# Optimization experiments

Hardware: AMD Instinct MI355X
Metric: run time of the kernel (lower is better)

Reference implementation:

```python
import jax, jax.numpy as jnp
import numpy as np

TAU = 2.0          # LIF membrane time constant (init kwarg)
ALPHA = 2.0        # spikingjelly surrogate.ATan default alpha
V_TH = 1.0         # spikingjelly LIFNode default v_threshold

# Heaviside spike with ATan surrogate gradient (spikingjelly semantics)
@jax.custom_vjp
def spike(v):
    return (v >= V_TH).astype(v.dtype)

def _spike_fwd(v):
    return spike(v), v

def _spike_bwd(v, g):
    sg = (ALPHA / 2.0) / (1.0 + (jnp.pi / 2.0 * ALPHA * (v - V_TH)) ** 2)
    return (g * sg,)

spike.defvjp(_spike_fwd, _spike_bwd)

def lif(x):
    # Fresh LIFNode: v_prev = 0, v_reset = 0, decay_input=True
    # charge: v = v_prev + (x - (v_prev - v_reset)) / tau  ->  v = x / tau
    return spike(x / TAU)

def setup_inputs() -> dict:
    key = jax.random.key(0)
    ks = jax.random.split(key, 5)
    B = 2097152
    # kaiming-uniform-ish scale: 1/sqrt(fan_in)
    def w(k, out_f, in_f):
        return jax.random.normal(k, (out_f, in_f), dtype=jnp.float32) / np.sqrt(in_f)
    return {
        "x": jax.random.normal(ks[0], (B, 5), dtype=jnp.float32),
        "W1": w(ks[1], 32, 5),
        "W2": w(ks[2], 32, 32),
        "W3": w(ks[3], 16, 32),
        "W4": w(ks[4], 10, 16),
    }

def reference(x, W1, W2, W3, W4):
    # fc: Linear(5,32)->LIF -> Linear(32,32)->LIF -> Linear(32,16)->LIF
    s = lif(x @ W1.T)          # [B, 32]
    s = lif(s @ W2.T)          # [B, 32]
    s = lif(s @ W3.T)          # [B, 16]
    # fc1: Linear(16,10)->LIF
    return lif(s @ W4.T)       # [B, 10]
```

## Files before the change

### kernel.cpp

```cpp
#include <hip/hip_runtime.h>


typedef float v4f __attribute__((ext_vector_type(4)));

#define RPB 256

__global__ __launch_bounds__(256, 8) void snn_fused(
    const float* __restrict__ x,
    const float* __restrict__ W1,
    const float* __restrict__ W2,
    const float* __restrict__ W3,
    const float* __restrict__ W4,
    float* __restrict__ out,
    int B)
{
    __shared__ __align__(16) float xbuf[RPB * 5];
    __shared__ __align__(16) float obuf[RPB * 10];
    __shared__ float smx[32];
    __shared__ float smxmax;

    const int t = threadIdx.x;
    const long base = (long)blockIdx.x * RPB;
    const int nrows = (int)min((long)RPB, (long)B - base);

    if (t < 32) {
        float mm = W2[t];
#pragma unroll
        for (int j = 1; j < 32; ++j) mm = fmaxf(mm, W2[j * 32 + t]);
        smx[t] = mm;
        float r = mm;
#pragma unroll
        for (int off = 16; off; off >>= 1) r = fmaxf(r, __shfl_xor(r, off, 32));
        if (t == 0) smxmax = r;
    }

    if (nrows == RPB) {
        const v4f* xg = (const v4f*)(x + base * 5);
        v4f* b4 = (v4f*)xbuf;
#pragma unroll
        for (int e = 0; e < 2; ++e) {
            int idx = e * 256 + t;
            if (idx < (RPB * 5) / 4) b4[idx] = xg[idx];
        }
    } else {
        for (int e = t; e < nrows * 5; e += 256) xbuf[e] = x[base * 5 + e];
    }
    __syncthreads();

    const float mxmax = smxmax;

    if (t < nrows) {
        float xr[5];
#pragma unroll
        for (int k = 0; k < 5; ++k) xr[k] = xbuf[t * 5 + k];

        unsigned m = 0u;
#pragma unroll
        for (int j = 0; j < 32; ++j) {
            const float* w = W1 + j * 5;
            float h = xr[0] * w[0];
            h += xr[1] * w[1];
            h += xr[2] * w[2];
            h += xr[3] * w[3];
            h += xr[4] * w[4];
            if (h >= 2.0f) m |= (1u << j);
        }

        float o[10];
#pragma unroll
        for (int j = 0; j < 10; ++j) o[j] = 0.0f;

        if ((float)__popc(m) * mxmax >= 1.998f) {
            float S = 0.0f;
            unsigned mm = m;
            while (mm) { int i = __ffs(mm) - 1; mm &= mm - 1; S += smx[i]; }
            if (S >= 1.998f) {
                float h2[32];
#pragma unroll
                for (int j = 0; j < 32; ++j) h2[j] = 0.0f;
                mm = m;
                while (mm) {
                    int i = __ffs(mm) - 1;
                    mm &= mm - 1;
                    const float* col = W2 + i;
#pragma unroll
                    for (int j = 0; j < 32; ++j) h2[j] += col[j * 32];
                }
                unsigned m2 = 0u;
#pragma unroll
                for (int j = 0; j < 32; ++j)
                    if (h2[j] >= 2.0f) m2 |= (1u << j);

                if (m2) {
                    unsigned m3 = 0u;
#pragma unroll
                    for (int j = 0; j < 16; ++j) {
                        float g = 0.0f;
#pragma unroll
                        for (int i = 0; i < 32; ++i)
                            if ((m2 >> i) & 1u) g += W3[j * 32 + i];
                        if (g >= 2.0f) m3 |= (1u << j);
                    }
#pragma unroll
                    for (int j = 0; j < 10; ++j) {
                        float g = 0.0f;
#pragma unroll
                        for (int i = 0; i < 16; ++i)
                            if ((m3 >> i) & 1u) g += W4[j * 16 + i];
                        o[j] = (g >= 2.0f) ? 1.0f : 0.0f;
                    }
                }
            }
        }

#pragma unroll
        for (int j = 0; j < 10; ++j) obuf[t * 10 + j] = o[j];
    }
    __syncthreads();

    if (nrows == RPB) {
        v4f* og = (v4f*)(out + base * 10);
        const v4f* b4 = (const v4f*)obuf;
#pragma unroll
        for (int e = 0; e < 3; ++e) {
            int idx = e * 256 + t;
            if (idx < (RPB * 10) / 4)
                __builtin_nontemporal_store(b4[idx], &og[idx]);
        }
    } else {
        for (int e = t; e < nrows * 10; e += 256) out[base * 10 + e] = obuf[e];
    }
}

extern "C" void kernel_launch(void* const* d_in, const int* in_sizes, int n_in,
                              void* d_out, int out_size, void* d_ws, size_t ws_size,
                              hipStream_t stream) {
    const float* x  = (const float*)d_in[0];
    const float* W1 = (const float*)d_in[1];
    const float* W2 = (const float*)d_in[2];
    const float* W3 = (const float*)d_in[3];
    const float* W4 = (const float*)d_in[4];
    float* out = (float*)d_out;

    int B = in_sizes[0] / 5;
    int grid = (B + RPB - 1) / RPB;
    snn_fused<<<grid, 256, 0, stream>>>(x, W1, W2, W3, W4, out, B);
}
```

Before: 156.7 us.

## Process four rows per thread with prep kernel and wave-level shuffle screening

Adds a tiny prep kernel that transposes W1 into a workspace and precomputes per-column maxima of W2, so each main block no longer recomputes them. The main kernel now has each thread handle four rows, loaded and stored directly with vector accesses, replacing the shared-memory staging and both __syncthreads. Layer 1 uses packed float2 multiply-adds. The S screening sum uses wave-wide shuffles instead of shared-memory lookups. The costs are an extra kernel launch, higher register pressure, and fewer threads in flight with four times fewer blocks.

```diff
diff --git a/kernel.cpp b/kernel.cpp
--- a/kernel.cpp
+++ b/kernel.cpp
@@ -2,85 +2,109 @@
 
 
 typedef float v4f __attribute__((ext_vector_type(4)));
+typedef float v2f __attribute__((ext_vector_type(2)));
 
-#define RPB 256
+#define TPB 256
+#define RPL 4
+#define RPB (TPB * RPL)
 
-__global__ __launch_bounds__(256, 8) void snn_fused(
+__global__ __launch_bounds__(64) void snn_prep(
+    const float* __restrict__ W1,
+    const float* __restrict__ W2,
+    float* __restrict__ ws)
+{
+    const int t = threadIdx.x;
+    float mm = -3.4e38f;
+    if (t < 32) {
+#pragma unroll
+        for (int k = 0; k < 5; ++k) ws[k * 32 + t] = W1[t * 5 + k];
+        mm = W2[t];
+#pragma unroll
+        for (int j = 1; j < 32; ++j) mm = fmaxf(mm, W2[j * 32 + t]);
+        ws[160 + t] = mm;
+    }
+#pragma unroll
+    for (int off = 32; off; off >>= 1) mm = fmaxf(mm, __shfl_xor(mm, off));
+    if (t == 0) ws[192] = mm;
+}
+
+__global__ __launch_bounds__(TPB) void snn_fused(
     const float* __restrict__ x,
-    const float* __restrict__ W1,
     const float* __restrict__ W2,
     const float* __restrict__ W3,
     const float* __restrict__ W4,
+    const float* __restrict__ ws,
     float* __restrict__ out,
     int B)
 {
-    __shared__ __align__(16) float xbuf[RPB * 5];
-    __shared__ __align__(16) float obuf[RPB * 10];
-    __shared__ float smx[32];
-    __shared__ float smxmax;
+    const long gtid = (long)blockIdx.x * TPB + threadIdx.x;
+    const long r0 = gtid * RPL;
+    if (r0 >= B) return;
+    const bool full = (r0 + RPL <= B);
 
-    const int t = threadIdx.x;
-    const long base = (long)blockIdx.x * RPB;
-    const int nrows = (int)min((long)RPB, (long)B - base);
+    const v2f* __restrict__ w1p = (const v2f*)ws;
+    const float smxv = ws[160 + (threadIdx.x & 31)];
+    const float mxmax = ws[192];
 
-    if (t < 32) {
-        float mm = W2[t];
+    __align__(16) float xf[RPL * 5];
+    if (full) {
+        const v4f* xg = (const v4f*)(x + r0 * 5);
+        v4f* xv = (v4f*)xf;
 #pragma unroll
-        for (int j = 1; j < 32; ++j) mm = fmaxf(mm, W2[j * 32 + t]);
-        smx[t] = mm;
-        float r = mm;
+        for (int e = 0; e < 5; ++e) xv[e] = xg[e];
+    } else {
 #pragma unroll
-        for (int off = 16; off; off >>= 1) r = fmaxf(r, __shfl_xor(r, off, 32));
-        if (t == 0) smxmax = r;
+        for (int e = 0; e < RPL * 5; ++e) xf[e] = 0.0f;
+        for (int c = 0; c < RPL; ++c)
+            if (r0 + c < B)
+#pragma unroll
+                for (int k = 0; k < 5; ++k) xf[c * 5 + k] = x[(r0 + c) * 5 + k];
     }
 
-    if (nrows == RPB) {
-        const v4f* xg = (const v4f*)(x + base * 5);
-        v4f* b4 = (v4f*)xbuf;
+    __align__(16) float o[RPL * 10];
 #pragma unroll
-        for (int e = 0; e < 2; ++e) {
-            int idx = e * 256 + t;
-            if (idx < (RPB * 5) / 4) b4[idx] = xg[idx];
-        }
-    } else {
-        for (int e = t; e < nrows * 5; e += 256) xbuf[e] = x[base * 5 + e];
-    }
-    __syncthreads();
+    for (int e = 0; e < RPL * 10; ++e) o[e] = 0.0f;
 
-    const float mxmax = smxmax;
+#pragma unroll
+    for (int c = 0; c < RPL; ++c) {
+        const float x0 = xf[c * 5 + 0], x1 = xf[c * 5 + 1], x2 = xf[c * 5 + 2];
+        const float x3 = xf[c * 5 + 3], x4 = xf[c * 5 + 4];
 
-    if (t < nrows) {
-        float xr[5];
+        v2f hp[16];
 #pragma unroll
-        for (int k = 0; k < 5; ++k) xr[k] = xbuf[t * 5 + k];
+        for (int j2 = 0; j2 < 16; ++j2) hp[j2] = x0 * w1p[j2];
+#pragma unroll
+        for (int j2 = 0; j2 < 16; ++j2) hp[j2] += x1 * w1p[16 + j2];
+#pragma unroll
+        for (int j2 = 0; j2 < 16; ++j2) hp[j2] += x2 * w1p[32 + j2];
+#pragma unroll
+        for (int j2 = 0; j2 < 16; ++j2) hp[j2] += x3 * w1p[48 + j2];
+#pragma unroll
+        for (int j2 = 0; j2 < 16; ++j2) hp[j2] += x4 * w1p[64 + j2];
 
         unsigned m = 0u;
 #pragma unroll
-        for (int j = 0; j < 32; ++j) {
-            const float* w = W1 + j * 5;
-            float h = xr[0] * w[0];
-            h += xr[1] * w[1];
-            h += xr[2] * w[2];
-            h += xr[3] * w[3];
-            h += xr[4] * w[4];
-            if (h >= 2.0f) m |= (1u << j);
+        for (int j2 = 0; j2 < 16; ++j2) {
+            if (hp[j2].x >= 2.0f) m |= (1u << (2 * j2));
+            if (hp[j2].y >= 2.0f) m |= (1u << (2 * j2 + 1));
         }
 
-        float o[10];
-#pragma unroll
-        for (int j = 0; j < 10; ++j) o[j] = 0.0f;
-
-        if ((float)__popc(m) * mxmax >= 1.998f) {
+        const bool need = m && ((float)__popc(m) * mxmax >= 1.998f);
+        if (__any(need)) {
             float S = 0.0f;
-            unsigned mm = m;
-            while (mm) { int i = __ffs(mm) - 1; mm &= mm - 1; S += smx[i]; }
-            if (S >= 1.998f) {
+            unsigned mm = need ? m : 0u;
+            while (__any(mm)) {
+                const int i = mm ? (__ffs(mm) - 1) : 0;
+                const float v = __shfl(smxv, i);
+                if (mm) { S += v; mm &= mm - 1; }
+            }
+            if (need && S >= 1.998f) {
                 float h2[32];
 #pragma unroll
                 for (int j = 0; j < 32; ++j) h2[j] = 0.0f;
                 mm = m;
                 while (mm) {
-                    int i = __ffs(mm) - 1;
+                    const int i = __ffs(mm) - 1;
                     mm &= mm - 1;
                     const float* col = W2 + i;
 #pragma unroll
@@ -107,28 +131,23 @@
 #pragma unroll
                         for (int i = 0; i < 16; ++i)
                             if ((m3 >> i) & 1u) g += W4[j * 16 + i];
-                        o[j] = (g >= 2.0f) ? 1.0f : 0.0f;
+                        o[c * 10 + j] = (g >= 2.0f) ? 1.0f : 0.0f;
                     }
                 }
             }
         }
+    }
 
+    if (full) {
+        v4f* og = (v4f*)(out + r0 * 10);
+        const v4f* o4 = (const v4f*)o;
 #pragma unroll
-        for (int j = 0; j < 10; ++j) obuf[t * 10 + j] = o[j];
-    }
-    __syncthreads();
-
-    if (nrows == RPB) {
-        v4f* og = (v4f*)(out + base * 10);
-        const v4f* b4 = (const v4f*)obuf;
+        for (int e = 0; e < 10; ++e) __builtin_nontemporal_store(o4[e], &og[e]);
+    } else {
+        for (int c = 0; c < RPL; ++c)
+            if (r0 + c < B)
 #pragma unroll
-        for (int e = 0; e < 3; ++e) {
-            int idx = e * 256 + t;
-            if (idx < (RPB * 10) / 4)
-                __builtin_nontemporal_store(b4[idx], &og[idx]);
-        }
-    } else {
-        for (int e = t; e < nrows * 10; e += 256) out[base * 10 + e] = obuf[e];
+                for (int j = 0; j < 10; ++j) out[(r0 + c) * 10 + j] = o[c * 10 + j];
     }
 }
 
@@ -141,8 +160,10 @@
     const float* W3 = (const float*)d_in[3];
     const float* W4 = (const float*)d_in[4];
     float* out = (float*)d_out;
+    float* ws  = (float*)d_ws;
 
     int B = in_sizes[0] / 5;
+    snn_prep<<<1, 64, 0, stream>>>(W1, W2, ws);
     int grid = (B + RPB - 1) / RPB;
-    snn_fused<<<grid, 256, 0, stream>>>(x, W1, W2, W3, W4, out, B);
+    snn_fused<<<grid, TPB, 0, stream>>>(x, W2, W3, W4, ws, out, B);
 }
```

Measured after the change: 326.6 us. +108.5%, slower.
